# Kernel optimization log

Hardware: AMD Instinct MI355X
Metric: run time of the kernel (lower is better)

Reference implementation:

```python
import jax, jax.numpy as jnp
import numpy as np

EMBED_DIM = 2048
NUM_HEADS = 16
HEAD_DIM = EMBED_DIM // NUM_HEADS
EPS = 1e-6


def setup_inputs() -> dict:
    key = jax.random.key(0)
    ks = jax.random.split(key, 12)
    B, S, D = 4, 2048, EMBED_DIM
    s = 1.0 / np.sqrt(D)
    return {
        "query": jax.random.normal(ks[0], (B, S, D), jnp.float32),
        "key": jax.random.normal(ks[1], (B, S, D), jnp.float32),
        "value": jax.random.normal(ks[2], (B, S, D), jnp.float32),
        "Wq": jax.random.normal(ks[3], (D, D), jnp.float32) * s,
        "bq": jnp.zeros((D,), jnp.float32),
        "Wk": jax.random.normal(ks[4], (D, D), jnp.float32) * s,
        "bk": jnp.zeros((D,), jnp.float32),
        "Wv": jax.random.normal(ks[5], (D, D), jnp.float32) * s,
        "bv": jnp.zeros((D,), jnp.float32),
        "Wo": jax.random.normal(ks[6], (D, D), jnp.float32) * s,
        "bo": jnp.zeros((D,), jnp.float32),
        "q_norm_w": jnp.ones((HEAD_DIM,), jnp.float32),
        "k_norm_w": jnp.ones((HEAD_DIM,), jnp.float32),
    }


def _rms_norm(x, w):
    # RMSNorm over last dim (head_dim): x / sqrt(mean(x^2)+eps) * w
    ms = jnp.mean(jnp.square(x), axis=-1, keepdims=True)
    return x * jax.lax.rsqrt(ms + EPS) * w


def reference(query, key, value, Wq, bq, Wk, bk, Wv, bv, Wo, bo, q_norm_w, k_norm_w):
    B, Nq, D = query.shape
    Nk = key.shape[1]
    H, Hd = NUM_HEADS, HEAD_DIM
    # torch nn.Linear: y = x @ W.T + b
    q = (query @ Wq.T + bq).reshape(B, Nq, H, Hd).transpose(0, 2, 1, 3)  # (B,H,Nq,Hd)
    k = (key @ Wk.T + bk).reshape(B, Nk, H, Hd).transpose(0, 2, 1, 3)
    v = (value @ Wv.T + bv).reshape(B, Nk, H, Hd).transpose(0, 2, 1, 3)
    q = _rms_norm(q, q_norm_w)
    k = _rms_norm(k, k_norm_w)
    scale = 1.0 / np.sqrt(Hd)
    scores = jnp.einsum("bhqd,bhkd->bhqk", q, k) * scale  # (B,H,Nq,Nk)
    attn = jax.nn.softmax(scores, axis=-1)
    out = jnp.einsum("bhqk,bhkd->bhqd", attn, v)  # (B,H,Nq,Hd)
    out = out.transpose(0, 2, 1, 3).reshape(B, Nq, D)
    return out @ Wo.T + bo
```

## Files before the change

### kernel.cpp

```cpp
#include <hip/hip_runtime.h>

#define NB 4
#define NS 2048
#define ND 2048
#define NH 16
#define NHD 128

typedef __bf16 bf16;
typedef __attribute__((ext_vector_type(8))) __bf16 bf16x8;
typedef __attribute__((ext_vector_type(4))) __bf16 bf16x4;
typedef __attribute__((ext_vector_type(4))) float f32x4;

#define MFMA(a, b, c) __builtin_amdgcn_mfma_f32_16x16x32_bf16(a, b, c, 0, 0, 0)

__device__ __forceinline__ void gload16(const bf16* g, bf16* l) {
    __builtin_amdgcn_global_load_lds(
        (const __attribute__((address_space(1))) void*)g,
        (__attribute__((address_space(3))) void*)l, 16, 0, 0);
}

#define BAR() do { asm volatile("" ::: "memory"); __builtin_amdgcn_s_barrier(); \
                   asm volatile("" ::: "memory"); } while (0)
#define VMCNT4() asm volatile("s_waitcnt vmcnt(4)" ::: "memory")

enum { RA00 = 0, RA01 = 16384, RA10 = 32768, RA11 = 49152,
       RB00 = 65536, RB01 = 81920, RB10 = 98304, RB11 = 114688 };

__device__ __forceinline__ void stage_half(const bf16* gcorner, char* lds_region,
                                           int w, int lane, int scol) {
    const bf16* g = gcorner + (size_t)(w * 16 + (lane >> 3)) * ND + scol;
    gload16(g, (bf16*)(lds_region + w * 2048));
    gload16(g + (size_t)8 * ND, (bf16*)(lds_region + w * 2048 + 1024));
}

__device__ __forceinline__ void lds_loadA(const char* pool, int region, int mi0,
                                          int l15, int quad, bf16x8 (&af)[8]) {
    const int flip = (l15 & 4) << 3;
    #pragma unroll
    for (int mi = 0; mi < 4; ++mi) {
        const int rb = region + ((mi0 + mi) * 16 + l15) * 128;
        #pragma unroll
        for (int kk = 0; kk < 2; ++kk)
            af[mi * 2 + kk] = *reinterpret_cast<const bf16x8*>(
                pool + rb + ((kk * 64 + quad * 16) ^ flip));
    }
}

template <int NI0>
__device__ __forceinline__ void lds_loadB(const char* pool, int region, int wn1,
                                          int l15, int quad, bf16x8 (&bfr)[8]) {
    const int flip = (l15 & 4) << 3;
    #pragma unroll
    for (int ni = 0; ni < 2; ++ni) {
        const int rb = region + (wn1 * 64 + (NI0 + ni) * 16 + l15) * 128;
        #pragma unroll
        for (int kk = 0; kk < 2; ++kk)
            bfr[(NI0 + ni) * 2 + kk] = *reinterpret_cast<const bf16x8*>(
                pool + rb + ((kk * 64 + quad * 16) ^ flip));
    }
}

template <int MI0, int NI0>
__device__ __forceinline__ void mfma_quad(f32x4 (&acc)[8][4], const bf16x8 (&af)[8],
                                          const bf16x8 (&bfr)[8]) {
    __builtin_amdgcn_s_setprio(1);
    #pragma unroll
    for (int mi = 0; mi < 4; ++mi)
        #pragma unroll
        for (int ni = 0; ni < 2; ++ni)
            #pragma unroll
            for (int kk = 0; kk < 2; ++kk)
                acc[MI0 + mi][NI0 + ni] =
                    MFMA(af[mi * 2 + kk], bfr[(NI0 + ni) * 2 + kk], acc[MI0 + mi][NI0 + ni]);
    __builtin_amdgcn_s_setprio(0);
}

#define GEMM256_KLOOP(Ab, Bb)                                                        \
    stage_half(Ab, pool + RA00, w, lane, scol);                                      \
    stage_half(Ab + (size_t)128 * ND, pool + RA01, w, lane, scol);                   \
    stage_half(Bb, pool + RB00, w, lane, scol);                                      \
    stage_half(Bb + (size_t)128 * ND, pool + RB01, w, lane, scol);                   \
    stage_half(Bb + 64, pool + RB10, w, lane, scol);                                 \
    stage_half(Bb + (size_t)128 * ND + 64, pool + RB11, w, lane, scol);              \
    VMCNT4();                                                                        \
    BAR();                                                                           \
    for (int i = 0; i < 16; ++i) {                                                   \
        const int kA = (2 * i + 1) * 64;                                             \
        const int kN = (2 * i + 2) * 64;                                             \
        const int kN3 = (2 * i + 3) * 64;                                            \
                                                                             \
        lds_loadA(pool, rA0, 0, l15, quad, af);                                      \
        lds_loadB<0>(pool, rB0, wn1, l15, quad, bfr);                                \
        stage_half(Ab + kA, pool + RA10, w, lane, scol);                             \
        BAR(); mfma_quad<0, 0>(acc, af, bfr); BAR();                                 \
                                                                             \
        lds_loadB<2>(pool, rB0, wn1, l15, quad, bfr);                                \
        stage_half(Ab + (size_t)128 * ND + kA, pool + RA11, w, lane, scol);          \
        BAR(); mfma_quad<0, 2>(acc, af, bfr); BAR();                                 \
                                                                             \
        lds_loadA(pool, rA0, 4, l15, quad, af);                                      \
        stage_half(Bb + kN, pool + RB00, w, lane, scol);                             \
        BAR(); mfma_quad<4, 0>(acc, af, bfr); BAR();                                 \
                                                                             \
        stage_half(Bb + (size_t)128 * ND + kN, pool + RB01, w, lane, scol);          \
        VMCNT4();                                                                    \
        BAR(); mfma_quad<4, 2>(acc, af, bfr); BAR();                                 \
                                                                             \
        lds_loadA(pool, rA1, 0, l15, quad, af);                                      \
        lds_loadB<0>(pool, rB1, wn1, l15, quad, bfr);                                \
        stage_half(Ab + kN, pool + RA00, w, lane, scol);                             \
        BAR(); mfma_quad<0, 0>(acc, af, bfr); BAR();                                 \
                                                                             \
        lds_loadB<2>(pool, rB1, wn1, l15, quad, bfr);                                \
        stage_half(Ab + (size_t)128 * ND + kN, pool + RA01, w, lane, scol);          \
        BAR(); mfma_quad<0, 2>(acc, af, bfr); BAR();                                 \
                                                                             \
        lds_loadA(pool, rA1, 4, l15, quad, af);                                      \
        stage_half(Bb + kN3, pool + RB10, w, lane, scol);                            \
        BAR(); mfma_quad<4, 0>(acc, af, bfr); BAR();                                 \
                                                                             \
        stage_half(Bb + (size_t)128 * ND + kN3, pool + RB11, w, lane, scol);         \
        VMCNT4();                                                                    \
        BAR(); mfma_quad<4, 2>(acc, af, bfr); BAR();                                 \
    }

__global__ __launch_bounds__(256) void cvt_bf16(const float* __restrict__ src,
                                                bf16* __restrict__ dst)
{
    size_t i = ((size_t)blockIdx.x * 256 + threadIdx.x) * 8;
    float4 a = *reinterpret_cast<const float4*>(src + i);
    float4 b = *reinterpret_cast<const float4*>(src + i + 4);
    bf16x8 o;
    o[0] = (bf16)a.x; o[1] = (bf16)a.y; o[2] = (bf16)a.z; o[3] = (bf16)a.w;
    o[4] = (bf16)b.x; o[5] = (bf16)b.y; o[6] = (bf16)b.z; o[7] = (bf16)b.w;
    *reinterpret_cast<bf16x8*>(dst + i) = o;
}

__global__ __launch_bounds__(512, 2) void qkv_gemm(
    const bf16* __restrict__ Xb, const bf16* __restrict__ Wb,
    const float* __restrict__ bq, const float* __restrict__ bk, const float* __restrict__ bv,
    const float* __restrict__ qw, const float* __restrict__ kw,
    bf16* __restrict__ Oq, bf16* __restrict__ Ok, bf16* __restrict__ Ov)
{
    const int mat = blockIdx.z;
    const bf16* X     = Xb + (size_t)mat * (size_t)NB * NS * ND;
    const bf16* W     = Wb + (size_t)mat * ND * ND;
    const float* bias = (mat == 0) ? bq : (mat == 1) ? bk : bv;
    const float* nw   = (mat == 0) ? qw : kw;
    bf16* Out         = (mat == 0) ? Oq : (mat == 1) ? Ok : Ov;

    __shared__ alignas(1024) char pool[131072];
    __shared__ float red[256][4];
    __shared__ float scl[256][2];

    const int tid  = threadIdx.x;
    const int lane = tid & 63;
    const int w    = tid >> 6;
    const int wm   = w >> 2;
    const int wn   = w & 3;
    const int wn1  = wn & 1;
    const int quad = lane >> 4, l15 = lane & 15;

    const int m0 = blockIdx.y * 256;
    const int n0 = blockIdx.x * 256;

    const int scol = ((lane & 7) * 8) ^ ((lane & 32) ? 16 : 0);

    const int rA0 = RA00 + wm * 16384;
    const int rA1 = RA10 + wm * 16384;
    const int rB0 = RB00 + (wn >> 1) * 16384;
    const int rB1 = RB10 + (wn >> 1) * 16384;

    const bf16* Ab = X + (size_t)m0 * ND;
    const bf16* Bb = W + (size_t)n0 * ND;

    f32x4 acc[8][4] = {};
    bf16x8 af[8], bfr[8];

    GEMM256_KLOOP(Ab, Bb)

    #pragma unroll
    for (int ni = 0; ni < 4; ++ni) {
        float bn = bias[n0 + wn * 64 + ni * 16 + l15];
        #pragma unroll
        for (int mi = 0; mi < 8; ++mi)
            #pragma unroll
            for (int r = 0; r < 4; ++r)
                acc[mi][ni][r] += bn;
    }

    if (mat == 2) {
        bf16 (*Ts)[264] = (bf16(*)[264])pool;
        const int bb = m0 >> 11;
        const int s0 = m0 & (NS - 1);
        #pragma unroll
        for (int h2 = 0; h2 < 2; ++h2) {
            __syncthreads();
            if ((wn >> 1) == h2) {
                #pragma unroll
                for (int mi = 0; mi < 8; ++mi)
                    #pragma unroll
                    for (int ni = 0; ni < 4; ++ni) {
                        bf16x4 t;
                        #pragma unroll
                        for (int r = 0; r < 4; ++r) t[r] = (bf16)acc[mi][ni][r];
                        *reinterpret_cast<bf16x4*>(
                            &Ts[wn1 * 64 + ni * 16 + l15][wm * 128 + mi * 16 + quad * 4]) = t;
                    }
            }
            __syncthreads();
            const size_t obase = ((size_t)bb * NH + (n0 >> 7) + h2) * (size_t)NHD * NS;
            #pragma unroll
            for (int it = 0; it < 8; ++it) {
                int d = it * 16 + (tid >> 5);
                int c = (tid & 31) * 8;
                *reinterpret_cast<bf16x8*>(Out + obase + (size_t)d * NS + s0 + c) =
                    *reinterpret_cast<const bf16x8*>(&Ts[d][c]);
            }
        }
        return;
    }

    #pragma unroll
    for (int mi = 0; mi < 8; ++mi) {
        float ss[4];
        #pragma unroll
        for (int r = 0; r < 4; ++r) {
            float s = 0.f;
            #pragma unroll
            for (int ni = 0; ni < 4; ++ni) { float v = acc[mi][ni][r]; s += v * v; }
            ss[r] = s;
        }
        #pragma unroll
        for (int off = 1; off < 16; off <<= 1)
            #pragma unroll
            for (int r = 0; r < 4; ++r)
                ss[r] += __shfl_xor(ss[r], off);
        if (l15 == 0) {
            #pragma unroll
            for (int r = 0; r < 4; ++r)
                red[wm * 128 + mi * 16 + quad * 4 + r][wn] = ss[r];
        }
    }
    __syncthreads();
    {
        int row = tid >> 1, h2 = tid & 1;
        scl[row][h2] = rsqrtf((red[row][2 * h2] + red[row][2 * h2 + 1]) * (1.0f / 128.0f) + 1e-6f);
    }
    __syncthreads();

    const int hh = (n0 >> 7) + (wn >> 1);
    #pragma unroll
    for (int mi = 0; mi < 8; ++mi) {
        #pragma unroll
        for (int r = 0; r < 4; ++r) {
            int row = wm * 128 + mi * 16 + quad * 4 + r;
            int mg  = m0 + row;
            int bb  = mg >> 11;
            int ssi = mg & (NS - 1);
            size_t base = (((size_t)bb * NH + hh) * NS + ssi) * NHD;
            float sc_r = scl[row][wn >> 1];
            #pragma unroll
            for (int ni = 0; ni < 4; ++ni) {
                int col = (wn * 64 + ni * 16 + l15) & 127;
                Out[base + col] = (bf16)(acc[mi][ni][r] * sc_r * nw[col]);
            }
        }
    }
}

__global__ __launch_bounds__(256, 4) void flash_attn(
    const bf16* __restrict__ Q, const bf16* __restrict__ K, const bf16* __restrict__ Vt,
    bf16* __restrict__ O)
{
    __shared__ alignas(16) char apool[17408];
    __shared__ bf16 VtS[128][72];
    bf16 (*Ks)[136] = (bf16(*)[136])apool;
    bf16 (*Ps)[72]  = (bf16(*)[72])apool;

    const int tid  = threadIdx.x;
    const int lane = tid & 63;
    const int w    = tid >> 6;
    const int quad = lane >> 4, l15 = lane & 15;
    const int b    = blockIdx.z, h = blockIdx.y;
    const int q0   = blockIdx.x * 64;
    const size_t hb = ((size_t)b * NH + h) * (size_t)NS * NHD;
    const bf16* Qh  = Q + hb;
    const bf16* Kh  = K + hb;
    const bf16* Vth = Vt + hb;

    bf16x8 qf[4];
    #pragma unroll
    for (int ks = 0; ks < 4; ++ks)
        qf[ks] = *reinterpret_cast<const bf16x8*>(
            Qh + (size_t)(q0 + w * 16 + l15) * NHD + ks * 32 + quad * 8);

    const int kr = tid >> 4, kc = (tid & 15) * 8;
    const int vr = tid >> 3, vc = (tid & 7) * 8;
    const bf16* kp = Kh + (size_t)kr * NHD + kc;
    const bf16* vp = Vth + (size_t)vr * NS + vc;

    f32x4 o[8] = {};
    float m_r = -1e30f, l_r = 0.f;
    const float C = 0.12751740f;

    bf16x8 kreg[4], vreg[4];
    #pragma unroll
    for (int i = 0; i < 4; ++i)
        kreg[i] = *reinterpret_cast<const bf16x8*>(kp + (size_t)i * 16 * NHD);
    #pragma unroll
    for (int i = 0; i < 4; ++i)
        vreg[i] = *reinterpret_cast<const bf16x8*>(vp + (size_t)i * 32 * NS);
    #pragma unroll
    for (int i = 0; i < 4; ++i)
        *reinterpret_cast<bf16x8*>(&Ks[kr + i * 16][kc]) = kreg[i];
    #pragma unroll
    for (int i = 0; i < 4; ++i)
        *reinterpret_cast<bf16x8*>(&VtS[vr + i * 32][vc]) = vreg[i];
    __syncthreads();

    for (int kt = 0; kt < NS / 64; ++kt) {
        f32x4 sacc[4] = {};
        __builtin_amdgcn_s_setprio(1);
        #pragma unroll
        for (int ks = 0; ks < 4; ++ks) {
            #pragma unroll
            for (int kb = 0; kb < 4; ++kb) {
                bf16x8 kf = *reinterpret_cast<const bf16x8*>(&Ks[kb * 16 + l15][ks * 32 + quad * 8]);
                sacc[kb] = MFMA(kf, qf[ks], sacc[kb]);
            }
        }
        __builtin_amdgcn_s_setprio(0);

        if (kt + 1 < NS / 64) {
            kp += (size_t)64 * NHD;
            vp += 64;
            #pragma unroll
            for (int i = 0; i < 4; ++i)
                kreg[i] = *reinterpret_cast<const bf16x8*>(kp + (size_t)i * 16 * NHD);
            #pragma unroll
            for (int i = 0; i < 4; ++i)
                vreg[i] = *reinterpret_cast<const bf16x8*>(vp + (size_t)i * 32 * NS);
        }

        float t0 = fmaxf(fmaxf(sacc[0][0], sacc[0][1]), fmaxf(sacc[0][2], sacc[0][3]));
        float t1 = fmaxf(fmaxf(sacc[1][0], sacc[1][1]), fmaxf(sacc[1][2], sacc[1][3]));
        float t2 = fmaxf(fmaxf(sacc[2][0], sacc[2][1]), fmaxf(sacc[2][2], sacc[2][3]));
        float t3 = fmaxf(fmaxf(sacc[3][0], sacc[3][1]), fmaxf(sacc[3][2], sacc[3][3]));
        float mt = fmaxf(fmaxf(t0, t1), fmaxf(t2, t3));
        mt = fmaxf(mt, __shfl_xor(mt, 16));
        mt = fmaxf(mt, __shfl_xor(mt, 32));

        const bool grow = !__all(mt - m_r <= 64.0f);
        float alpha = 1.f;
        if (grow) {
            float mn = fmaxf(m_r, mt);
            alpha = __builtin_amdgcn_exp2f((m_r - mn) * C);
            m_r = mn;
        }
        const float mC = m_r * C;
        float rsk[4];
        #pragma unroll
        for (int kb = 0; kb < 4; ++kb) {
            #pragma unroll
            for (int r = 0; r < 4; ++r)
                sacc[kb][r] = __builtin_amdgcn_exp2f(sacc[kb][r] * C - mC);
            rsk[kb] = (sacc[kb][0] + sacc[kb][1]) + (sacc[kb][2] + sacc[kb][3]);
        }
        float rs = (rsk[0] + rsk[1]) + (rsk[2] + rsk[3]);
        rs += __shfl_xor(rs, 16);
        rs += __shfl_xor(rs, 32);
        l_r = l_r * alpha + rs;

        __syncthreads();

        #pragma unroll
        for (int kb = 0; kb < 4; ++kb) {
            bf16x4 t;
            #pragma unroll
            for (int r = 0; r < 4; ++r) t[r] = (bf16)sacc[kb][r];
            *reinterpret_cast<bf16x4*>(&Ps[w * 16 + l15][kb * 16 + quad * 4]) = t;
        }

        if (grow) {
            float alr[4];
            #pragma unroll
            for (int r = 0; r < 4; ++r) alr[r] = __shfl(alpha, quad * 4 + r);
            #pragma unroll
            for (int ci = 0; ci < 8; ++ci)
                #pragma unroll
                for (int r = 0; r < 4; ++r) o[ci][r] *= alr[r];
        }

        __builtin_amdgcn_s_setprio(1);
        #pragma unroll
        for (int ks = 0; ks < 2; ++ks) {
            bf16x8 a = *reinterpret_cast<const bf16x8*>(&Ps[w * 16 + l15][ks * 32 + quad * 8]);
            #pragma unroll
            for (int ci = 0; ci < 8; ++ci) {
                bf16x8 bb = *reinterpret_cast<const bf16x8*>(&VtS[ci * 16 + l15][ks * 32 + quad * 8]);
                o[ci] = MFMA(a, bb, o[ci]);
            }
        }
        __builtin_amdgcn_s_setprio(0);

        __syncthreads();

        if (kt + 1 < NS / 64) {
            #pragma unroll
            for (int i = 0; i < 4; ++i)
                *reinterpret_cast<bf16x8*>(&Ks[kr + i * 16][kc]) = kreg[i];
            #pragma unroll
            for (int i = 0; i < 4; ++i)
                *reinterpret_cast<bf16x8*>(&VtS[vr + i * 32][vc]) = vreg[i];
            __syncthreads();
        }
    }

    float lr_o[4];
    #pragma unroll
    for (int r = 0; r < 4; ++r) lr_o[r] = __shfl(l_r, quad * 4 + r);
    #pragma unroll
    for (int r = 0; r < 4; ++r) {
        int sg = q0 + w * 16 + quad * 4 + r;
        float inv = 1.0f / lr_o[r];
        size_t base = ((size_t)b * NS + sg) * ND + (size_t)h * NHD;
        #pragma unroll
        for (int ci = 0; ci < 8; ++ci)
            O[base + ci * 16 + l15] = (bf16)(o[ci][r] * inv);
    }
}

__global__ __launch_bounds__(512, 2) void oproj_gemm(
    const bf16* __restrict__ A, const bf16* __restrict__ Wt,
    const float* __restrict__ bias, float* __restrict__ Out)
{
    __shared__ alignas(1024) char pool[131072];

    const int tid  = threadIdx.x;
    const int lane = tid & 63;
    const int w    = tid >> 6;
    const int wm   = w >> 2;
    const int wn   = w & 3;
    const int wn1  = wn & 1;
    const int quad = lane >> 4, l15 = lane & 15;

    const int m0 = blockIdx.y * 256;
    const int n0 = blockIdx.x * 256;

    const int scol = ((lane & 7) * 8) ^ ((lane & 32) ? 16 : 0);

    const int rA0 = RA00 + wm * 16384;
    const int rA1 = RA10 + wm * 16384;
    const int rB0 = RB00 + (wn >> 1) * 16384;
    const int rB1 = RB10 + (wn >> 1) * 16384;

    const bf16* Ab = A + (size_t)m0 * ND;
    const bf16* Bb = Wt + (size_t)n0 * ND;

    f32x4 acc[8][4] = {};
    bf16x8 af[8], bfr[8];

    GEMM256_KLOOP(Ab, Bb)

    #pragma unroll
    for (int ni = 0; ni < 4; ++ni) {
        int colg = n0 + wn * 64 + ni * 16 + l15;
        float bn = bias[colg];
        #pragma unroll
        for (int mi = 0; mi < 8; ++mi)
            #pragma unroll
            for (int r = 0; r < 4; ++r) {
                int mg = m0 + wm * 128 + mi * 16 + quad * 4 + r;
                Out[(size_t)mg * ND + colg] = acc[mi][ni][r] + bn;
            }
    }
}

extern "C" void kernel_launch(void* const* d_in, const int* in_sizes, int n_in,
                              void* d_out, int out_size, void* d_ws, size_t ws_size,
                              hipStream_t stream)
{
    const float* q  = (const float*)d_in[0];
    const float* k  = (const float*)d_in[1];
    const float* v  = (const float*)d_in[2];
    const float* Wq = (const float*)d_in[3];
    const float* bq = (const float*)d_in[4];
    const float* Wk = (const float*)d_in[5];
    const float* bk = (const float*)d_in[6];
    const float* Wv = (const float*)d_in[7];
    const float* bv = (const float*)d_in[8];
    const float* Wo = (const float*)d_in[9];
    const float* bo = (const float*)d_in[10];
    const float* qw = (const float*)d_in[11];
    const float* kw = (const float*)d_in[12];
    float* out = (float*)d_out;

    const size_t nX = (size_t)NB * NS * ND;
    const size_t nW = (size_t)ND * ND;

    bf16* Xb  = (bf16*)d_ws;
    bf16* Wb  = Xb + 3 * nX;
    bf16* Qn  = Wb + 4 * nW;
    bf16* Kn  = Qn + nX;
    bf16* Vtp = Kn + nX;
    bf16* Ob  = Xb;

    cvt_bf16<<<8192, 256, 0, stream>>>(q,  Xb);
    cvt_bf16<<<8192, 256, 0, stream>>>(k,  Xb + nX);
    cvt_bf16<<<8192, 256, 0, stream>>>(v,  Xb + 2 * nX);
    cvt_bf16<<<2048, 256, 0, stream>>>(Wq, Wb);
    cvt_bf16<<<2048, 256, 0, stream>>>(Wk, Wb + nW);
    cvt_bf16<<<2048, 256, 0, stream>>>(Wv, Wb + 2 * nW);
    cvt_bf16<<<2048, 256, 0, stream>>>(Wo, Wb + 3 * nW);

    qkv_gemm<<<dim3(8, 32, 3), dim3(512), 0, stream>>>(
        Xb, Wb, bq, bk, bv, qw, kw, Qn, Kn, Vtp);
    flash_attn<<<dim3(32, 16, 4), dim3(256), 0, stream>>>(Qn, Kn, Vtp, Ob);
    oproj_gemm<<<dim3(8, 32), dim3(512), 0, stream>>>(Ob, Wb + 3 * nW, bo, out);
}
```

Measured before the change: 775.5 us.

## Restructure flash attention with 32x32 MFMA, larger query tiles, async double-buffered K/V

Rewrites the attention kernel so each 512-thread block handles 256 queries, with 32 per wave, using 32x32x16 bf16 MFMAs. K and V tiles are staged straight into swizzled LDS with global_load_lds and double-buffered, so loading the next tile overlaps compute and the register round-trip is gone. Each wave gets its own P buffer, which cuts the per-iteration barriers to roughly one. The cost is fewer blocks (512 instead of 2048), more LDS per block (96 KB) and larger accumulators, which may lower occupancy.

```diff
diff --git a/kernel.cpp b/kernel.cpp
--- a/kernel.cpp
+++ b/kernel.cpp
@@ -10,8 +10,10 @@
 typedef __attribute__((ext_vector_type(8))) __bf16 bf16x8;
 typedef __attribute__((ext_vector_type(4))) __bf16 bf16x4;
 typedef __attribute__((ext_vector_type(4))) float f32x4;
+typedef __attribute__((ext_vector_type(16))) float f32x16;
 
 #define MFMA(a, b, c) __builtin_amdgcn_mfma_f32_16x16x32_bf16(a, b, c, 0, 0, 0)
+#define MFMA32(a, b, c) __builtin_amdgcn_mfma_f32_32x32x16_bf16(a, b, c, 0, 0, 0)
 
 __device__ __forceinline__ void gload16(const bf16* g, bf16* l) {
     __builtin_amdgcn_global_load_lds(
@@ -22,6 +24,7 @@
 #define BAR() do { asm volatile("" ::: "memory"); __builtin_amdgcn_s_barrier(); \
                    asm volatile("" ::: "memory"); } while (0)
 #define VMCNT4() asm volatile("s_waitcnt vmcnt(4)" ::: "memory")
+#define VMCNT0() asm volatile("s_waitcnt vmcnt(0)" ::: "memory")
 
 enum { RA00 = 0, RA01 = 16384, RA10 = 32768, RA11 = 49152,
        RB00 = 65536, RB01 = 81920, RB10 = 98304, RB11 = 114688 };
@@ -269,86 +272,94 @@
     }
 }
 
-__global__ __launch_bounds__(256, 4) void flash_attn(
+__global__ __launch_bounds__(512, 2) void flash_attn(
     const bf16* __restrict__ Q, const bf16* __restrict__ K, const bf16* __restrict__ Vt,
     bf16* __restrict__ O)
 {
-    __shared__ alignas(16) char apool[17408];
-    __shared__ bf16 VtS[128][72];
-    bf16 (*Ks)[136] = (bf16(*)[136])apool;
-    bf16 (*Ps)[72]  = (bf16(*)[72])apool;
+    __shared__ alignas(1024) char kpool[32768];
+    __shared__ alignas(1024) char vpool[32768];
+    __shared__ alignas(1024) char ppool[32768];
 
     const int tid  = threadIdx.x;
     const int lane = tid & 63;
     const int w    = tid >> 6;
-    const int quad = lane >> 4, l15 = lane & 15;
+    const int l31  = lane & 31;
+    const int hi   = lane >> 5;
     const int b    = blockIdx.z, h = blockIdx.y;
-    const int q0   = blockIdx.x * 64;
+    const int q0   = blockIdx.x * 256;
     const size_t hb = ((size_t)b * NH + h) * (size_t)NS * NHD;
     const bf16* Qh  = Q + hb;
     const bf16* Kh  = K + hb;
     const bf16* Vth = Vt + hb;
 
-    bf16x8 qf[4];
-    #pragma unroll
-    for (int ks = 0; ks < 4; ++ks)
-        qf[ks] = *reinterpret_cast<const bf16x8*>(
-            Qh + (size_t)(q0 + w * 16 + l15) * NHD + ks * 32 + quad * 8);
-
-    const int kr = tid >> 4, kc = (tid & 15) * 8;
-    const int vr = tid >> 3, vc = (tid & 7) * 8;
-    const bf16* kp = Kh + (size_t)kr * NHD + kc;
-    const bf16* vp = Vth + (size_t)vr * NS + vc;
-
-    f32x4 o[8] = {};
+    bf16x8 qf[8];
+    {
+        const bf16* qrow = Qh + (size_t)(q0 + w * 32 + l31) * NHD + hi * 8;
+        #pragma unroll
+        for (int ks = 0; ks < 8; ++ks)
+            qf[ks] = *reinterpret_cast<const bf16x8*>(qrow + ks * 16);
+    }
+
+    char* Psb = ppool + w * 4096;
+    const int swz = (l31 & 7) << 4;
+    const int qrow_b = l31 * 128;
+
+    f32x16 o0 = {}, o1 = {}, o2 = {}, o3 = {};
     float m_r = -1e30f, l_r = 0.f;
     const float C = 0.12751740f;
 
-    bf16x8 kreg[4], vreg[4];
-    #pragma unroll
-    for (int i = 0; i < 4; ++i)
-        kreg[i] = *reinterpret_cast<const bf16x8*>(kp + (size_t)i * 16 * NHD);
-    #pragma unroll
-    for (int i = 0; i < 4; ++i)
-        vreg[i] = *reinterpret_cast<const bf16x8*>(vp + (size_t)i * 32 * NS);
-    #pragma unroll
-    for (int i = 0; i < 4; ++i)
-        *reinterpret_cast<bf16x8*>(&Ks[kr + i * 16][kc]) = kreg[i];
-    #pragma unroll
-    for (int i = 0; i < 4; ++i)
-        *reinterpret_cast<bf16x8*>(&VtS[vr + i * 32][vc]) = vreg[i];
-    __syncthreads();
-
-    for (int kt = 0; kt < NS / 64; ++kt) {
-        f32x4 sacc[4] = {};
+    auto stage_tile = [&](int t, int bufsel) {
+        const bf16* Kt  = Kh  + (size_t)(t & 31) * 64 * NHD;
+        const bf16* Vtt = Vth + (size_t)(t & 31) * 64;
+        char* Kb = kpool + bufsel * 16384;
+        char* Vb = vpool + bufsel * 16384;
+        #pragma unroll
+        for (int j = 0; j < 2; ++j) {
+            int c = w * 2 + j;
+            int krow  = 4 * c + (lane >> 4);
+            int kslot = (lane & 15) ^ (4 * (c & 1) + (lane >> 4));
+            gload16(Kt + (size_t)krow * NHD + kslot * 8, (bf16*)(Kb + c * 1024));
+            int vrow  = 8 * c + (lane >> 3);
+            int vslot = (lane & 7) ^ (lane >> 3);
+            gload16(Vtt + (size_t)vrow * NS + vslot * 8, (bf16*)(Vb + c * 1024));
+        }
+    };
+
+    stage_tile(0, 0);
+
+    const int NT = NS / 64;
+    for (int kt = 0; kt < NT; ++kt) {
+        const int cur = kt & 1;
+        if (kt + 1 < NT) {
+            stage_tile(kt + 1, cur ^ 1);
+            VMCNT4();
+        } else {
+            VMCNT0();
+        }
+        BAR();
+
+        const char* Kb = kpool + cur * 16384;
+        const char* Vb = vpool + cur * 16384;
+
+        f32x16 s0 = {}, s1 = {};
         __builtin_amdgcn_s_setprio(1);
         #pragma unroll
-        for (int ks = 0; ks < 4; ++ks) {
-            #pragma unroll
-            for (int kb = 0; kb < 4; ++kb) {
-                bf16x8 kf = *reinterpret_cast<const bf16x8*>(&Ks[kb * 16 + l15][ks * 32 + quad * 8]);
-                sacc[kb] = MFMA(kf, qf[ks], sacc[kb]);
-            }
+        for (int ks = 0; ks < 8; ++ks) {
+            const int co = ks * 32 + hi * 16;
+            bf16x8 k0 = *reinterpret_cast<const bf16x8*>(
+                Kb + l31 * 256 + (co ^ swz));
+            bf16x8 k1 = *reinterpret_cast<const bf16x8*>(
+                Kb + (32 + l31) * 256 + (co ^ swz));
+            s0 = MFMA32(k0, qf[ks], s0);
+            s1 = MFMA32(k1, qf[ks], s1);
         }
         __builtin_amdgcn_s_setprio(0);
 
-        if (kt + 1 < NS / 64) {
-            kp += (size_t)64 * NHD;
-            vp += 64;
-            #pragma unroll
-            for (int i = 0; i < 4; ++i)
-                kreg[i] = *reinterpret_cast<const bf16x8*>(kp + (size_t)i * 16 * NHD);
-            #pragma unroll
-            for (int i = 0; i < 4; ++i)
-                vreg[i] = *reinterpret_cast<const bf16x8*>(vp + (size_t)i * 32 * NS);
-        }
-
-        float t0 = fmaxf(fmaxf(sacc[0][0], sacc[0][1]), fmaxf(sacc[0][2], sacc[0][3]));
-        float t1 = fmaxf(fmaxf(sacc[1][0], sacc[1][1]), fmaxf(sacc[1][2], sacc[1][3]));
-        float t2 = fmaxf(fmaxf(sacc[2][0], sacc[2][1]), fmaxf(sacc[2][2], sacc[2][3]));
-        float t3 = fmaxf(fmaxf(sacc[3][0], sacc[3][1]), fmaxf(sacc[3][2], sacc[3][3]));
-        float mt = fmaxf(fmaxf(t0, t1), fmaxf(t2, t3));
-        mt = fmaxf(mt, __shfl_xor(mt, 16));
+        float mt = s0[0];
+        #pragma unroll
+        for (int r = 1; r < 16; ++r) mt = fmaxf(mt, s0[r]);
+        #pragma unroll
+        for (int r = 0; r < 16; ++r) mt = fmaxf(mt, s1[r]);
         mt = fmaxf(mt, __shfl_xor(mt, 32));
 
         const bool grow = !__all(mt - m_r <= 64.0f);
@@ -359,75 +370,63 @@
             m_r = mn;
         }
         const float mC = m_r * C;
-        float rsk[4];
-        #pragma unroll
-        for (int kb = 0; kb < 4; ++kb) {
-            #pragma unroll
-            for (int r = 0; r < 4; ++r)
-                sacc[kb][r] = __builtin_amdgcn_exp2f(sacc[kb][r] * C - mC);
-            rsk[kb] = (sacc[kb][0] + sacc[kb][1]) + (sacc[kb][2] + sacc[kb][3]);
-        }
-        float rs = (rsk[0] + rsk[1]) + (rsk[2] + rsk[3]);
-        rs += __shfl_xor(rs, 16);
+        float rs = 0.f;
+        #pragma unroll
+        for (int r = 0; r < 16; ++r) { s0[r] = __builtin_amdgcn_exp2f(s0[r] * C - mC); rs += s0[r]; }
+        #pragma unroll
+        for (int r = 0; r < 16; ++r) { s1[r] = __builtin_amdgcn_exp2f(s1[r] * C - mC); rs += s1[r]; }
         rs += __shfl_xor(rs, 32);
         l_r = l_r * alpha + rs;
 
-        __syncthreads();
-
-        #pragma unroll
-        for (int kb = 0; kb < 4; ++kb) {
-            bf16x4 t;
-            #pragma unroll
-            for (int r = 0; r < 4; ++r) t[r] = (bf16)sacc[kb][r];
-            *reinterpret_cast<bf16x4*>(&Ps[w * 16 + l15][kb * 16 + quad * 4]) = t;
+        #pragma unroll
+        for (int g = 0; g < 4; ++g) {
+            bf16x4 t0, t1;
+            #pragma unroll
+            for (int j = 0; j < 4; ++j) {
+                t0[j] = (bf16)s0[g * 4 + j];
+                t1[j] = (bf16)s1[g * 4 + j];
+            }
+            *reinterpret_cast<bf16x4*>(Psb + qrow_b + ((g * 16 + hi * 8) ^ swz)) = t0;
+            *reinterpret_cast<bf16x4*>(Psb + qrow_b + ((64 + g * 16 + hi * 8) ^ swz)) = t1;
         }
 
         if (grow) {
-            float alr[4];
-            #pragma unroll
-            for (int r = 0; r < 4; ++r) alr[r] = __shfl(alpha, quad * 4 + r);
-            #pragma unroll
-            for (int ci = 0; ci < 8; ++ci)
-                #pragma unroll
-                for (int r = 0; r < 4; ++r) o[ci][r] *= alr[r];
+            #pragma unroll
+            for (int r = 0; r < 16; ++r) {
+                float av = __shfl(alpha, (r & 3) + 8 * (r >> 2) + 4 * hi);
+                o0[r] *= av; o1[r] *= av; o2[r] *= av; o3[r] *= av;
+            }
         }
 
         __builtin_amdgcn_s_setprio(1);
         #pragma unroll
-        for (int ks = 0; ks < 2; ++ks) {
-            bf16x8 a = *reinterpret_cast<const bf16x8*>(&Ps[w * 16 + l15][ks * 32 + quad * 8]);
-            #pragma unroll
-            for (int ci = 0; ci < 8; ++ci) {
-                bf16x8 bb = *reinterpret_cast<const bf16x8*>(&VtS[ci * 16 + l15][ks * 32 + quad * 8]);
-                o[ci] = MFMA(a, bb, o[ci]);
-            }
+        for (int ks = 0; ks < 4; ++ks) {
+            const int co = ks * 32 + hi * 16;
+            bf16x8 pa = *reinterpret_cast<const bf16x8*>(Psb + qrow_b + (co ^ swz));
+            bf16x8 v0 = *reinterpret_cast<const bf16x8*>(Vb + l31 * 128 + (co ^ swz));
+            bf16x8 v1 = *reinterpret_cast<const bf16x8*>(Vb + (32 + l31) * 128 + (co ^ swz));
+            bf16x8 v2 = *reinterpret_cast<const bf16x8*>(Vb + (64 + l31) * 128 + (co ^ swz));
+            bf16x8 v3 = *reinterpret_cast<const bf16x8*>(Vb + (96 + l31) * 128 + (co ^ swz));
+            o0 = MFMA32(pa, v0, o0);
+            o1 = MFMA32(pa, v1, o1);
+            o2 = MFMA32(pa, v2, o2);
+            o3 = MFMA32(pa, v3, o3);
         }
         __builtin_amdgcn_s_setprio(0);
 
-        __syncthreads();
-
-        if (kt + 1 < NS / 64) {
-            #pragma unroll
-            for (int i = 0; i < 4; ++i)
-                *reinterpret_cast<bf16x8*>(&Ks[kr + i * 16][kc]) = kreg[i];
-            #pragma unroll
-            for (int i = 0; i < 4; ++i)
-                *reinterpret_cast<bf16x8*>(&VtS[vr + i * 32][vc]) = vreg[i];
-            __syncthreads();
-        }
-    }
-
-    float lr_o[4];
-    #pragma unroll
-    for (int r = 0; r < 4; ++r) lr_o[r] = __shfl(l_r, quad * 4 + r);
-    #pragma unroll
-    for (int r = 0; r < 4; ++r) {
-        int sg = q0 + w * 16 + quad * 4 + r;
-        float inv = 1.0f / lr_o[r];
-        size_t base = ((size_t)b * NS + sg) * ND + (size_t)h * NHD;
-        #pragma unroll
-        for (int ci = 0; ci < 8; ++ci)
-            O[base + ci * 16 + l15] = (bf16)(o[ci][r] * inv);
+        BAR();
+    }
+
+    #pragma unroll
+    for (int r = 0; r < 16; ++r) {
+        int qp = (r & 3) + 8 * (r >> 2) + 4 * hi;
+        float inv = 1.0f / __shfl(l_r, qp);
+        int sg = q0 + w * 32 + qp;
+        size_t base = ((size_t)b * NS + sg) * ND + (size_t)h * NHD + l31;
+        O[base]      = (bf16)(o0[r] * inv);
+        O[base + 32] = (bf16)(o1[r] * inv);
+        O[base + 64] = (bf16)(o2[r] * inv);
+        O[base + 96] = (bf16)(o3[r] * inv);
     }
 }
 
@@ -516,6 +515,6 @@
 
     qkv_gemm<<<dim3(8, 32, 3), dim3(512), 0, stream>>>(
         Xb, Wb, bq, bk, bv, qw, kw, Qn, Kn, Vtp);
-    flash_attn<<<dim3(32, 16, 4), dim3(256), 0, stream>>>(Qn, Kn, Vtp, Ob);
+    flash_attn<<<dim3(8, 16, 4), dim3(512), 0, stream>>>(Qn, Kn, Vtp, Ob);
     oproj_gemm<<<dim3(8, 32), dim3(512), 0, stream>>>(Ob, Wb + 3 * nW, bo, out);
 }
```

Measured after the change: 739.2 us. 4.7% less time.
